# Kernel optimization log

Measured on AMD Instinct MI355X. Metric: run time of the kernel, lower is better.

Reference implementation:

```python
import jax, jax.numpy as jnp
import numpy as np

D = 1024      # neural_dim
M = 8192      # memory_size (assumed fully used)
H = 16        # num_heads
B = 64        # batch
HD = D // H   # head dim


def setup_inputs() -> dict:
    key = jax.random.key(0)
    ks = jax.random.split(key, 24)
    s = 0.02
    inp = {
        "neural_input": jax.random.normal(ks[0], (B, D), jnp.float32),
        "memory_keys": jax.random.normal(ks[1], (M, D), jnp.float32),
        "memory_values": jax.random.normal(ks[2], (M, D), jnp.float32),
        # query/key/value projections (nn.Linear weights are [out, in])
        "Wq": jax.random.normal(ks[3], (D, D), jnp.float32) * s,
        "bq": jnp.zeros((D,), jnp.float32),
        "Wk": jax.random.normal(ks[4], (D, D), jnp.float32) * s,
        "bk": jnp.zeros((D,), jnp.float32),
        "Wv": jax.random.normal(ks[5], (D, D), jnp.float32) * s,
        "bv": jnp.zeros((D,), jnp.float32),
        # MultiheadAttention packed in-projection [3D, D] and out projection
        "in_proj_w": jax.random.normal(ks[6], (3 * D, D), jnp.float32) * s,
        "in_proj_b": jnp.zeros((3 * D,), jnp.float32),
        "out_w": jax.random.normal(ks[7], (D, D), jnp.float32) * s,
        "out_b": jnp.zeros((D,), jnp.float32),
        # memory_gate: Linear(2D->D), ReLU, Linear(D->D), Sigmoid
        "gW1": jax.random.normal(ks[8], (D, 2 * D), jnp.float32) * s,
        "gb1": jnp.zeros((D,), jnp.float32),
        "gW2": jax.random.normal(ks[9], (D, D), jnp.float32) * s,
        "gb2": jnp.zeros((D,), jnp.float32),
        # integration: Linear(2D->2D), ReLU, Linear(2D->D)
        "iW1": jax.random.normal(ks[10], (2 * D, 2 * D), jnp.float32) * s,
        "ib1": jnp.zeros((2 * D,), jnp.float32),
        "iW2": jax.random.normal(ks[11], (D, 2 * D), jnp.float32) * s,
        "ib2": jnp.zeros((D,), jnp.float32),
    }
    return inp


def reference(neural_input, memory_keys, memory_values,
              Wq, bq, Wk, bk, Wv, bv,
              in_proj_w, in_proj_b, out_w, out_b,
              gW1, gb1, gW2, gb2, iW1, ib1, iW2, ib2):
    x = neural_input  # [B, D]
    # pre-projections (memory_used assumed all True -> full tables)
    q = x @ Wq.T + bq                  # [B, D]
    k = memory_keys @ Wk.T + bk        # [M, D]
    v = memory_values @ Wv.T + bv      # [M, D]

    # MultiheadAttention (single query per batch element; K/V shared
    # across batch instead of the redundant expand in the original)
    Wiq, Wik, Wiv = in_proj_w[:D], in_proj_w[D:2 * D], in_proj_w[2 * D:]
    biq, bik, biv = in_proj_b[:D], in_proj_b[D:2 * D], in_proj_b[2 * D:]
    qh = (q @ Wiq.T + biq).reshape(B, H, HD)   # [B, H, hd]
    kh = (k @ Wik.T + bik).reshape(M, H, HD)   # [M, H, hd]
    vh = (v @ Wiv.T + biv).reshape(M, H, HD)   # [M, H, hd]

    scale = 1.0 / np.sqrt(HD).astype(np.float32)
    scores = jnp.einsum('bhd,mhd->bhm', qh, kh) * scale  # [B, H, M]
    attn = jax.nn.softmax(scores, axis=-1)
    ctx = jnp.einsum('bhm,mhd->bhd', attn, vh).reshape(B, D)
    memory_signal = ctx @ out_w.T + out_b      # [B, D]

    # gated fusion
    gate_in = jnp.concatenate([x, memory_signal], axis=-1)          # [B, 2D]
    gate = jax.nn.sigmoid(jax.nn.relu(gate_in @ gW1.T + gb1) @ gW2.T + gb2)
    gated_memory = gate * memory_signal
    combined = jnp.concatenate([x, gated_memory], axis=-1)          # [B, 2D]
    out = jax.nn.relu(combined @ iW1.T + ib1) @ iW2.T + ib2         # [B, D]
    return out
```

## Files before the change

### kernel.cpp

```cpp
#include <hip/hip_runtime.h>
#include <hip/hip_bf16.h>
#include <stdint.h>


typedef __bf16 bf16;
typedef __bf16 bf16x4 __attribute__((ext_vector_type(4)));
typedef __bf16 bf16x8 __attribute__((ext_vector_type(8)));
typedef float f32x4 __attribute__((ext_vector_type(4)));

#define D_ 1024
#define M_ 8192
#define B_ 64
#define H_ 16

static __device__ __forceinline__ void gload16(const void* g, void* l) {
  __builtin_amdgcn_global_load_lds(
      (const __attribute__((address_space(1))) void*)g,
      (__attribute__((address_space(3))) void*)l, 16, 0, 0);
}

static __device__ __forceinline__ f32x4 mfma16(bf16x8 a, bf16x8 b, f32x4 c) {
  return __builtin_amdgcn_mfma_f32_16x16x32_bf16(a, b, c, 0, 0, 0);
}

template <int U, int KLEN, typename OutT>
__device__ __forceinline__ void thin_gemm(
    const bf16* __restrict__ A, int lda,
    const bf16* __restrict__ Bm, int ldb,
    OutT* __restrict__ C, int ldc,
    const float* __restrict__ bias, float scale) {
  const int tid = threadIdx.x, lane = tid & 63, w = tid >> 6;
  const int rl = lane & 15, qq = lane >> 4;
  const bf16* pa = A + (int64_t)(w * 16 + rl) * lda + qq * 8;
  const bf16* pb[4];
  pb[0] = Bm + (int64_t)rl * ldb + qq * 8;
  pb[1] = pb[0] + (int64_t)16 * ldb;
  pb[2] = pb[0] + (int64_t)32 * ldb;
  pb[3] = pb[0] + (int64_t)48 * ldb;
  f32x4 acc[4] = {};
  bf16x8 av[2][U], bv[2][U][4];
#pragma unroll
  for (int u = 0; u < U; u++) {
    av[0][u] = *(const bf16x8*)(pa + u * 32);
#pragma unroll
    for (int j = 0; j < 4; j++)
      bv[0][u][j] = *(const bf16x8*)(pb[j] + u * 32);
  }
  constexpr int NI = KLEN / (32 * U);
#pragma unroll
  for (int it = 0; it < NI; it++) {
    const int cur = it & 1, nxt = cur ^ 1;
    if (it + 1 < NI) {
      int k = (it + 1) * 32 * U;
#pragma unroll
      for (int u = 0; u < U; u++) {
        av[nxt][u] = *(const bf16x8*)(pa + k + u * 32);
#pragma unroll
        for (int j = 0; j < 4; j++)
          bv[nxt][u][j] = *(const bf16x8*)(pb[j] + k + u * 32);
      }
    }
#pragma unroll
    for (int u = 0; u < U; u++)
#pragma unroll
      for (int j = 0; j < 4; j++)
        acc[j] = mfma16(av[cur][u], bv[cur][u][j], acc[j]);
  }
#pragma unroll
  for (int j = 0; j < 4; j++) {
    int gn = j * 16 + rl;
    float bb = bias ? bias[gn] : 0.0f;
#pragma unroll
    for (int r = 0; r < 4; r++) {
      int gm = w * 16 + qq * 4 + r;
      C[(int64_t)gm * ldc + gn] = (OutT)((acc[j][r] + bb) * scale);
    }
  }
}

struct CvtD { const float* src; bf16* dst; int end; };
struct PrepArgs {
  CvtD d[9];
  const float *Wq, *Wk, *Wv, *inw, *inb, *bq, *bk, *bv;
  const float *outb, *gb1, *gb2, *ib1, *ib2;
  bf16* WT;
  float *bc, *msR, *g1R, *gateR, *h1R, *out, *Oraw, *lmat;
};

__global__ __launch_bounds__(256) void prep_kernel(PrepArgs a) {
  const int bx = blockIdx.x, tid = threadIdx.x;
  if (bx < 29760) {
    int g = bx * 256 + tid;
    CvtD dd = a.d[8];
    int begin = a.d[7].end;
#pragma unroll
    for (int t = 7; t >= 0; t--)
      if (g < a.d[t].end) { dd = a.d[t]; begin = t ? a.d[t - 1].end : 0; }
    int i = (g - begin) * 4;
    float4 v = *(const float4*)(dd.src + i);
    bf16x4 o = { (bf16)v.x, (bf16)v.y, (bf16)v.z, (bf16)v.w };
    *(bf16x4*)(dd.dst + i) = o;
  } else if (bx < 32832) {
    int t = bx - 29760;
    int z = t >> 10, rem = t & 1023;
    const float* src = z == 0 ? a.Wq : z == 1 ? a.Wk : a.Wv;
    bf16* out = a.WT + (int64_t)z * D_ * D_;
    __shared__ bf16 tile[32][33];
    int tx = tid & 31, ty = tid >> 5;
    int r0 = (rem >> 5) * 32, c0 = (rem & 31) * 32;
#pragma unroll
    for (int i = 0; i < 32; i += 8)
      tile[ty + i][tx] = (bf16)src[(int64_t)(r0 + ty + i) * D_ + c0 + tx];
    __syncthreads();
#pragma unroll
    for (int i = 0; i < 32; i += 8)
      out[(int64_t)(c0 + ty + i) * D_ + r0 + tx] = tile[tx][ty + i];
  } else if (bx < 33600) {
    int t = bx - 32832;
    int w = tid >> 6, lane = tid & 63;
    int ng = t * 4 + w;
    int z = ng >> 10;
    const float* Wi = a.inw + (int64_t)ng * D_;
    const float* b = z == 0 ? a.bq : z == 1 ? a.bk : a.bv;
    float acc = 0.f;
#pragma unroll
    for (int l = 0; l < D_; l += 64) acc += Wi[l + lane] * b[l + lane];
#pragma unroll
    for (int m = 32; m; m >>= 1) acc += __shfl_xor(acc, m, 64);
    if (lane == 0) a.bc[ng] = acc + a.inb[ng];
  } else if (bx < 33984) {
    int t = bx - 33600;
    int seg = t >> 6, row = t & 63;
    int n = tid * 4;
    const float* b;
    float* dst;
    int bn = n;
    if (seg == 0)      { dst = a.msR   + row * 1024;        b = a.outb; }
    else if (seg == 1) { dst = a.g1R   + row * 1024;        b = a.gb1;  }
    else if (seg == 2) { dst = a.gateR + row * 1024;        b = a.gb2;  }
    else if (seg == 3) { dst = a.h1R   + row * 2048;        b = a.ib1;  }
    else if (seg == 4) { dst = a.h1R   + row * 2048 + 1024; b = a.ib1; bn = 1024 + n; }
    else               { dst = a.out   + row * 1024;        b = a.ib2;  }
    *(float4*)(dst + n) = *(const float4*)(b + bn);
  } else {
    int b = bx - 33984;
    float4 z4 = {0.f, 0.f, 0.f, 0.f};
    *(float4*)(a.Oraw + b * 1024 + tid * 4) = z4;
    if (b < 16 && tid < 64) a.lmat[b * 64 + tid] = 0.f;
  }
}

template <int MODE>
__global__ __launch_bounds__(256) void gemm_big(
    const bf16* __restrict__ A, int lda, int64_t sA,
    const bf16* __restrict__ Bm, int ldb, int64_t sB,
    bf16* __restrict__ C, int ldc, int64_t sC, bf16* __restrict__ Ct,
    const float* __restrict__ bias, int64_t sbias, int K,
    const bf16* __restrict__ qA, const bf16* __restrict__ qB,
    bf16* __restrict__ qC, const float* __restrict__ qbias) {
  int m0, n0, z;
  if (MODE == 0) {
    z = blockIdx.z; m0 = blockIdx.y * 128; n0 = blockIdx.x * 128;
  } else {
    if ((int)blockIdx.x >= 1024) {
      int n0q = ((int)blockIdx.x - 1024) * 64;
      thin_gemm<2, 1024, bf16>(qA, D_, qB + (int64_t)n0q * D_, D_,
                               qC + n0q, D_, qbias + n0q, 0.125f);
      return;
    }
    int lin = blockIdx.x, xcd = lin & 7, slot = lin >> 3;
    z = slot >> 6;
    int r = slot & 63;
    m0 = (xcd * 8 + (r >> 3)) * 128;
    n0 = (r & 7) * 128;
  }
  A += (int64_t)z * sA; Bm += (int64_t)z * sB;
  if (bias) bias += (int64_t)z * sbias;
  __shared__ alignas(16) bf16 As[128 * 32];
  __shared__ alignas(16) bf16 Bs[128 * 32];
  const int tid = threadIdx.x, lane = tid & 63, w = tid >> 6;
  const int wm = (w & 1) * 64, wn = (w >> 1) * 64;
  const int rl = lane & 15, qq = lane >> 4;
  f32x4 acc[4][4] = {};

  int c0 = w * 64 + lane, c1 = (4 + w) * 64 + lane;
  int ra0 = c0 >> 2, qa0 = (c0 & 3) ^ ((ra0 >> 1) & 3);
  int ra1 = c1 >> 2, qa1 = (c1 & 3) ^ ((ra1 >> 1) & 3);
  const bf16* gA0 = A + (int64_t)(m0 + ra0) * lda + qa0 * 8;
  const bf16* gA1 = A + (int64_t)(m0 + ra1) * lda + qa1 * 8;
  const bf16* gB0 = Bm + (int64_t)(n0 + ra0) * ldb + qa0 * 8;
  const bf16* gB1 = Bm + (int64_t)(n0 + ra1) * ldb + qa1 * 8;
  bf16* lA0 = As + w * 512;
  bf16* lA1 = As + (4 + w) * 512;
  bf16* lB0 = Bs + w * 512;
  bf16* lB1 = Bs + (4 + w) * 512;

  for (int k0 = 0; k0 < K; k0 += 32) {
    __syncthreads();
    gload16(gA0 + k0, lA0);
    gload16(gA1 + k0, lA1);
    gload16(gB0 + k0, lB0);
    gload16(gB1 + k0, lB1);
    __syncthreads();
    bf16x8 af[4], bb[4];
#pragma unroll
    for (int i = 0; i < 4; i++) {
      int r = wm + i * 16 + rl;
      af[i] = *(const bf16x8*)(As + r * 32 + (qq ^ ((r >> 1) & 3)) * 8);
    }
#pragma unroll
    for (int j = 0; j < 4; j++) {
      int r = wn + j * 16 + rl;
      bb[j] = *(const bf16x8*)(Bs + r * 32 + (qq ^ ((r >> 1) & 3)) * 8);
    }
#pragma unroll
    for (int i = 0; i < 4; i++)
#pragma unroll
      for (int j = 0; j < 4; j++)
        acc[i][j] = mfma16(af[i], bb[j], acc[i][j]);
  }
  if (MODE == 1 && z == 1) {
#pragma unroll
    for (int j = 0; j < 4; j++) {
      int gn = n0 + wn + j * 16 + rl;
      float bb2 = bias ? bias[gn] : 0.0f;
#pragma unroll
      for (int i = 0; i < 4; i++) {
        int gm0 = m0 + wm + i * 16 + qq * 4;
        f32x4 a = acc[i][j];
        bf16x4 o = { (bf16)(a[0] + bb2), (bf16)(a[1] + bb2),
                     (bf16)(a[2] + bb2), (bf16)(a[3] + bb2) };
        *(bf16x4*)(Ct + (int64_t)gn * M_ + gm0) = o;
      }
    }
  } else {
    C += (int64_t)z * sC;
#pragma unroll
    for (int j = 0; j < 4; j++) {
      int gn = n0 + wn + j * 16 + rl;
      float bb2 = bias ? bias[gn] : 0.0f;
#pragma unroll
      for (int i = 0; i < 4; i++) {
        int gm0 = m0 + wm + i * 16 + qq * 4;
#pragma unroll
        for (int r = 0; r < 4; r++)
          C[(int64_t)(gm0 + r) * ldc + gn] = (bf16)(acc[i][j][r] + bb2);
      }
    }
  }
}

__global__ __launch_bounds__(512) void gemm256(
    const bf16* __restrict__ A,
    const bf16* __restrict__ Wc,
    const float* __restrict__ bc,
    bf16* __restrict__ kh, bf16* __restrict__ vhT,
    const bf16* __restrict__ qA, const bf16* __restrict__ qB,
    bf16* __restrict__ qC, const float* __restrict__ qbias) {
  extern __shared__ __align__(16) bf16 lds[];
  const int bid = blockIdx.x;
  if (bid >= 256) {
    if (threadIdx.x < 256) {
      int n0q = (bid - 256) * 64;
      thin_gemm<2, 1024, bf16>(qA, D_, qB + (int64_t)n0q * D_, D_,
                               qC + n0q, D_, qbias + n0q, 0.125f);
    }
    return;
  }
  const int lin = bid;
  const int xcd = lin & 7, s = lin >> 3;
  const int z = xcd >> 2;
  const int m0 = ((xcd & 3) * 8 + (s >> 2)) * 256;
  const int n0 = (s & 3) * 256;
  const bf16* Ab = A + (int64_t)z * M_ * D_;
  const bf16* Bb = Wc + (int64_t)(z + 1) * D_ * D_;
  const float* bias = bc + (z + 1) * D_;

  const int tid = threadIdx.x, lane = tid & 63, w = tid >> 6;
  const int rl = lane & 15, qq = lane >> 4;
  const int wr = w >> 2, wcn = w & 3;

  const int ci0 = w * 128 + lane, ci1 = ci0 + 64;
  const int ra0 = ci0 >> 2, ca0 = (ci0 & 3) ^ ((ra0 >> 1) & 3);
  const int ra1 = ci1 >> 2, ca1 = (ci1 & 3) ^ ((ra1 >> 1) & 3);
  const bf16* gA0 = Ab + (int64_t)(m0 + ra0) * D_ + ca0 * 8;
  const bf16* gA1 = Ab + (int64_t)(m0 + ra1) * D_ + ca1 * 8;
  const bf16* gB0 = Bb + (int64_t)(n0 + ra0) * D_ + ca0 * 8;
  const bf16* gB1 = Bb + (int64_t)(n0 + ra1) * D_ + ca1 * 8;
  const int lA0 = w * 1024, lA1 = lA0 + 512;

  f32x4 acc[8][4] = {};
  bf16x8 bfr[4], afr[4];
  const int sq8 = (qq ^ ((rl >> 1) & 3)) * 8;

#define SCB __builtin_amdgcn_sched_barrier(0)
#define BARR __builtin_amdgcn_s_barrier()
#define VMW(N) asm volatile("s_waitcnt vmcnt(" #N ")")

#define STAGE_FULL(BUF, KT)                          \
  do {                                               \
    bf16* bse_ = lds + (BUF) * 16384;                \
    gload16(gA0 + (KT) * 32, bse_ + lA0);            \
    gload16(gA1 + (KT) * 32, bse_ + lA1);            \
    gload16(gB0 + (KT) * 32, bse_ + 8192 + lA0);     \
    gload16(gB1 + (KT) * 32, bse_ + 8192 + lA1);     \
  } while (0)

#define PH_A(BUF, DOSTAGE, SKT)                                              \
  do {                                                                       \
    const bf16* ba_ = lds + (BUF) * 16384;                                   \
    const bf16* bb_ = ba_ + 8192;                                            \
    for (int j = 0; j < 4; j++)                                              \
      bfr[j] = *(const bf16x8*)(bb_ + (wcn * 64 + j * 16 + rl) * 32 + sq8);  \
    for (int mi = 0; mi < 4; mi++)                                           \
      afr[mi] = *(const bf16x8*)(ba_ + (wr * 128 + mi * 16 + rl) * 32 + sq8);\
    if (DOSTAGE) {                                                           \
      bf16* bse_ = lds + ((SKT) & 3) * 16384;                                \
      gload16(gA0 + (SKT) * 32, bse_ + lA0);                                 \
      gload16(gA1 + (SKT) * 32, bse_ + lA1);                                 \
    }                                                                        \
    SCB; BARR; SCB;                                                          \
    __builtin_amdgcn_s_setprio(1);                                           \
    for (int mi = 0; mi < 4; mi++)                                           \
      for (int j = 0; j < 4; j++)                                            \
        acc[mi][j] = mfma16(afr[mi], bfr[j], acc[mi][j]);                    \
    __builtin_amdgcn_s_setprio(0);                                           \
    SCB; BARR; SCB;                                                          \
  } while (0)

#define PH_B(BUF, DOSTAGE, SKT, VMSTMT)                                      \
  do {                                                                       \
    const bf16* ba_ = lds + (BUF) * 16384;                                   \
    for (int mi = 0; mi < 4; mi++)                                           \
      afr[mi] =                                                              \
          *(const bf16x8*)(ba_ + (wr * 128 + (mi + 4) * 16 + rl) * 32 + sq8);\
    if (DOSTAGE) {                                                           \
      bf16* bse_ = lds + ((SKT) & 3) * 16384;                                \
      gload16(gB0 + (SKT) * 32, bse_ + 8192 + lA0);                          \
      gload16(gB1 + (SKT) * 32, bse_ + 8192 + lA1);                          \
    }                                                                        \
    VMSTMT;                                                                  \
    SCB; BARR; SCB;                                                          \
    __builtin_amdgcn_s_setprio(1);                                           \
    for (int mi = 0; mi < 4; mi++)                                           \
      for (int j = 0; j < 4; j++)                                            \
        acc[mi + 4][j] = mfma16(afr[mi], bfr[j], acc[mi + 4][j]);            \
    __builtin_amdgcn_s_setprio(0);                                           \
    SCB; BARR; SCB;                                                          \
  } while (0)

  STAGE_FULL(0, 0);
  STAGE_FULL(1, 1);
  STAGE_FULL(2, 2);
  VMW(8);
  SCB; BARR; SCB;

#pragma unroll 1
  for (int t = 0; t < 7; t++) {
    const int kb = t * 4;
    PH_A(0, 1, kb + 3); PH_B(0, 1, kb + 3, VMW(8));
    PH_A(1, 1, kb + 4); PH_B(1, 1, kb + 4, VMW(8));
    PH_A(2, 1, kb + 5); PH_B(2, 1, kb + 5, VMW(8));
    PH_A(3, 1, kb + 6); PH_B(3, 1, kb + 6, VMW(8));
  }
  PH_A(0, 1, 31); PH_B(0, 1, 31, VMW(8));
  PH_A(1, 0, 0);  PH_B(1, 0, 0, VMW(4));
  PH_A(2, 0, 0);  PH_B(2, 0, 0, VMW(0));
  PH_A(3, 0, 0);  PH_B(3, 0, 0, (void)0);

#undef SCB
#undef BARR
#undef VMW
#undef STAGE_FULL
#undef PH_A
#undef PH_B

  if (z == 0) {
#pragma unroll
    for (int j = 0; j < 4; j++) {
      int gn = n0 + wcn * 64 + j * 16 + rl;
      float bb2 = bias[gn];
#pragma unroll
      for (int mi = 0; mi < 8; mi++) {
        int gm0 = m0 + wr * 128 + mi * 16 + qq * 4;
#pragma unroll
        for (int r = 0; r < 4; r++)
          kh[(int64_t)(gm0 + r) * D_ + gn] = (bf16)(acc[mi][j][r] + bb2);
      }
    }
  } else {
#pragma unroll
    for (int j = 0; j < 4; j++) {
      int gn = n0 + wcn * 64 + j * 16 + rl;
      float bb2 = bias[gn];
#pragma unroll
      for (int mi = 0; mi < 8; mi++) {
        int gm0 = m0 + wr * 128 + mi * 16 + qq * 4;
        f32x4 a = acc[mi][j];
        bf16x4 o = { (bf16)(a[0] + bb2), (bf16)(a[1] + bb2),
                     (bf16)(a[2] + bb2), (bf16)(a[3] + bb2) };
        *(bf16x4*)(vhT + (int64_t)gn * M_ + gm0) = o;
      }
    }
  }
}

__global__ __launch_bounds__(256, 2) void flash_kernel(
    const bf16* __restrict__ qh, const bf16* __restrict__ kh,
    const bf16* __restrict__ vhT, float* __restrict__ Oraw,
    float* __restrict__ lmat) {
  const int tid = threadIdx.x, lane = tid & 63, w = tid >> 6;
  const int rl = lane & 15, qq = lane >> 4;
  const int h = blockIdx.x >> 4, c = blockIdx.x & 15;
  __shared__ alignas(16) bf16 Plds[4 * 16 * 72];
  const bf16* qhp = qh + (int64_t)(w * 16 + rl) * D_ + h * 64 + qq * 8;
  bf16x8 aq0 = *(const bf16x8*)(qhp);
  bf16x8 aq1 = *(const bf16x8*)(qhp + 32);
  float lsum[4] = {0.f, 0.f, 0.f, 0.f};
  f32x4 acc_o[4] = {};
  bf16* pl = Plds + w * 1152;
  const bf16* khb = kh + (int64_t)(c * 512) * D_ + h * 64 + qq * 8;
  const bf16* vtb = vhT + (int64_t)(h * 64) * M_ + c * 512 + qq * 8;
  for (int nt = 0; nt < 8; nt++) {
    int mb = nt * 64;
    bf16x8 bk0[4], bk1[4], vv0[4], vv1[4];
#pragma unroll
    for (int j = 0; j < 4; j++) {
      const bf16* p = khb + (int64_t)(mb + j * 16 + rl) * D_;
      bk0[j] = *(const bf16x8*)(p);
      bk1[j] = *(const bf16x8*)(p + 32);
      const bf16* q = vtb + (int64_t)(j * 16 + rl) * M_ + mb;
      vv0[j] = *(const bf16x8*)(q);
      vv1[j] = *(const bf16x8*)(q + 32);
    }
    f32x4 s[4] = {};
#pragma unroll
    for (int j = 0; j < 4; j++) {
      s[j] = mfma16(aq0, bk0[j], s[j]);
      s[j] = mfma16(aq1, bk1[j], s[j]);
    }
#pragma unroll
    for (int j = 0; j < 4; j++)
#pragma unroll
      for (int r = 0; r < 4; r++) {
        float p = __expf(s[j][r]);
        lsum[r] += p;
        pl[(qq * 4 + r) * 72 + j * 16 + rl] = (bf16)p;
      }
    bf16x8 pa0 = *(const bf16x8*)(pl + rl * 72 + qq * 8);
    bf16x8 pa1 = *(const bf16x8*)(pl + rl * 72 + 32 + qq * 8);
#pragma unroll
    for (int j = 0; j < 4; j++) {
      acc_o[j] = mfma16(pa0, vv0[j], acc_o[j]);
      acc_o[j] = mfma16(pa1, vv1[j], acc_o[j]);
    }
  }
#pragma unroll
  for (int msk = 1; msk <= 8; msk <<= 1)
#pragma unroll
    for (int r = 0; r < 4; r++) lsum[r] += __shfl_xor(lsum[r], msk, 64);
#pragma unroll
  for (int j = 0; j < 4; j++)
#pragma unroll
    for (int r = 0; r < 4; r++)
      atomicAdd(&Oraw[(int64_t)(w * 16 + qq * 4 + r) * D_ + h * 64 + j * 16 + rl],
                acc_o[j][r]);
  if (rl == 0)
#pragma unroll
    for (int r = 0; r < 4; r++)
      atomicAdd(&lmat[h * 64 + w * 16 + qq * 4 + r], lsum[r]);
}

struct Chunk { const void* p0; const void* p1; int ld; int kind; };
struct StageArgs { Chunk c[16]; };

template <int NKK>
__global__ __launch_bounds__(256) void tail_stage(
    StageArgs sa, const bf16* __restrict__ Bw, int ldb,
    float* __restrict__ Craw, int ldc) {
  const int n0 = blockIdx.x * 64, kc = blockIdx.y;
  const int bk0 = kc * NKK * 32;
  const Chunk ch = sa.c[kc];
  const int tid = threadIdx.x, lane = tid & 63, w = tid >> 6;
  const int rl = lane & 15, qq = lane >> 4;
  const int m = w * 16 + rl;
  const bf16* pb[4];
#pragma unroll
  for (int j = 0; j < 4; j++)
    pb[j] = Bw + (int64_t)(n0 + j * 16 + rl) * ldb + bk0 + qq * 8;
  f32x4 acc[4] = {};
#pragma unroll
  for (int kk = 0; kk < NKK; kk++) {
    bf16x8 af;
    if (ch.kind == 0) {
      af = *(const bf16x8*)((const bf16*)ch.p0 + (int64_t)m * ch.ld +
                            kk * 32 + qq * 8);
    } else {
      const float* p = (const float*)ch.p0 + (int64_t)m * ch.ld + kk * 32 + qq * 8;
      float4 u0 = *(const float4*)p;
      float4 u1 = *(const float4*)(p + 4);
      if (ch.kind == 2) {
        u0.x = fmaxf(u0.x, 0.f); u0.y = fmaxf(u0.y, 0.f);
        u0.z = fmaxf(u0.z, 0.f); u0.w = fmaxf(u0.w, 0.f);
        u1.x = fmaxf(u1.x, 0.f); u1.y = fmaxf(u1.y, 0.f);
        u1.z = fmaxf(u1.z, 0.f); u1.w = fmaxf(u1.w, 0.f);
      } else if (ch.kind == 3) {
        const float* pm = (const float*)ch.p1 + (int64_t)m * ch.ld + kk * 32 + qq * 8;
        float4 m0 = *(const float4*)pm;
        float4 m1 = *(const float4*)(pm + 4);
        u0.x = m0.x / (1.f + __expf(-u0.x)); u0.y = m0.y / (1.f + __expf(-u0.y));
        u0.z = m0.z / (1.f + __expf(-u0.z)); u0.w = m0.w / (1.f + __expf(-u0.w));
        u1.x = m1.x / (1.f + __expf(-u1.x)); u1.y = m1.y / (1.f + __expf(-u1.y));
        u1.z = m1.z / (1.f + __expf(-u1.z)); u1.w = m1.w / (1.f + __expf(-u1.w));
      } else if (ch.kind == 4) {
        int hidx = (bk0 + kk * 32) >> 6;
        float linv = 1.0f / ((const float*)ch.p1)[hidx * 64 + m];
        u0.x *= linv; u0.y *= linv; u0.z *= linv; u0.w *= linv;
        u1.x *= linv; u1.y *= linv; u1.z *= linv; u1.w *= linv;
      }
      af = (bf16x8){ (bf16)u0.x, (bf16)u0.y, (bf16)u0.z, (bf16)u0.w,
                     (bf16)u1.x, (bf16)u1.y, (bf16)u1.z, (bf16)u1.w };
    }
    bf16x8 bf_[4];
#pragma unroll
    for (int j = 0; j < 4; j++) bf_[j] = *(const bf16x8*)(pb[j] + kk * 32);
#pragma unroll
    for (int j = 0; j < 4; j++) acc[j] = mfma16(af, bf_[j], acc[j]);
  }
#pragma unroll
  for (int j = 0; j < 4; j++) {
    int gn = n0 + j * 16 + rl;
#pragma unroll
    for (int r = 0; r < 4; r++) {
      int gm = w * 16 + qq * 4 + r;
      atomicAdd(&Craw[(int64_t)gm * ldc + gn], acc[j][r]);
    }
  }
}

extern "C" void kernel_launch(void* const* d_in, const int* in_sizes, int n_in,
                              void* d_out, int out_size, void* d_ws,
                              size_t ws_size, hipStream_t stream) {
  (void)in_sizes; (void)n_in; (void)out_size;
  const float* x    = (const float*)d_in[0];
  const float* mk   = (const float*)d_in[1];
  const float* mv   = (const float*)d_in[2];
  const float* Wq   = (const float*)d_in[3];
  const float* bq   = (const float*)d_in[4];
  const float* Wk   = (const float*)d_in[5];
  const float* bk   = (const float*)d_in[6];
  const float* Wv   = (const float*)d_in[7];
  const float* bv   = (const float*)d_in[8];
  const float* inw  = (const float*)d_in[9];
  const float* inb  = (const float*)d_in[10];
  const float* outw = (const float*)d_in[11];
  const float* outb = (const float*)d_in[12];
  const float* gW1  = (const float*)d_in[13];
  const float* gb1  = (const float*)d_in[14];
  const float* gW2  = (const float*)d_in[15];
  const float* gb2  = (const float*)d_in[16];
  const float* iW1  = (const float*)d_in[17];
  const float* ib1  = (const float*)d_in[18];
  const float* iW2  = (const float*)d_in[19];
  const float* ib2  = (const float*)d_in[20];

  char* ws = (char*)d_ws;
  size_t off = 0;
  auto alloc = [&](size_t bytes) {
    char* p = ws + off;
    off += (bytes + 255) & ~(size_t)255;
    return p;
  };
  bf16* mkmv  = (bf16*)alloc((size_t)2 * M_ * D_ * 2);
  bf16* inpj  = (bf16*)alloc((size_t)3 * D_ * D_ * 2);
  bf16* WT    = (bf16*)alloc((size_t)3 * D_ * D_ * 2);
  bf16* Wc    = (bf16*)alloc((size_t)3 * D_ * D_ * 2);
  float* bc   = (float*)alloc(3 * D_ * 4);
  bf16* xbf   = (bf16*)alloc((size_t)B_ * D_ * 2);
  bf16* qh    = (bf16*)alloc((size_t)B_ * D_ * 2);
  bf16* kh    = (bf16*)alloc((size_t)M_ * D_ * 2);
  bf16* vhT   = (bf16*)alloc((size_t)M_ * D_ * 2);
  float* Oraw = (float*)alloc((size_t)B_ * D_ * 4);
  float* lmat = (float*)alloc((size_t)H_ * B_ * 4);
  float* msR  = (float*)alloc((size_t)B_ * D_ * 4);
  float* g1R  = (float*)alloc((size_t)B_ * D_ * 4);
  float* gateR= (float*)alloc((size_t)B_ * D_ * 4);
  float* h1R  = (float*)alloc((size_t)B_ * 2 * D_ * 4);
  bf16* gW1b  = (bf16*)alloc((size_t)D_ * 2 * D_ * 2);
  bf16* gW2b  = (bf16*)alloc((size_t)D_ * D_ * 2);
  bf16* iW1b  = (bf16*)alloc((size_t)2 * D_ * 2 * D_ * 2);
  bf16* iW2b  = (bf16*)alloc((size_t)D_ * 2 * D_ * 2);
  bf16* outwb = (bf16*)alloc((size_t)D_ * D_ * 2);
  if (ws_size < off) return;

  PrepArgs pa;
  pa.d[0] = { mk,   mkmv,           2097152 };
  pa.d[1] = { mv,   mkmv + M_ * D_, 4194304 };
  pa.d[2] = { inw,  inpj,           4980736 };
  pa.d[3] = { gW1,  gW1b,           5505024 };
  pa.d[4] = { gW2,  gW2b,           5767168 };
  pa.d[5] = { iW1,  iW1b,           6815744 };
  pa.d[6] = { iW2,  iW2b,           7340032 };
  pa.d[7] = { outw, outwb,          7602176 };
  pa.d[8] = { x,    xbf,            7618560 };
  pa.Wq = Wq; pa.Wk = Wk; pa.Wv = Wv; pa.inw = inw; pa.inb = inb;
  pa.bq = bq; pa.bk = bk; pa.bv = bv;
  pa.outb = outb; pa.gb1 = gb1; pa.gb2 = gb2; pa.ib1 = ib1; pa.ib2 = ib2;
  pa.WT = WT; pa.bc = bc; pa.msR = msR; pa.g1R = g1R; pa.gateR = gateR;
  pa.h1R = h1R; pa.out = (float*)d_out; pa.Oraw = Oraw; pa.lmat = lmat;
  prep_kernel<<<dim3(34048), 256, 0, stream>>>(pa);

  gemm_big<0><<<dim3(8, 8, 3), 256, 0, stream>>>(
      inpj, D_, (int64_t)D_ * D_, WT, D_, (int64_t)D_ * D_,
      Wc, D_, (int64_t)D_ * D_, nullptr, nullptr, 0, D_,
      nullptr, nullptr, nullptr, nullptr);

  hipFuncSetAttribute((const void*)gemm256,
                      hipFuncAttributeMaxDynamicSharedMemorySize, 131072);
  gemm256<<<dim3(272), dim3(512), 131072, stream>>>(
      mkmv, Wc, bc, kh, vhT, xbf, Wc, qh, bc);

  flash_kernel<<<dim3(256), 256, 0, stream>>>(qh, kh, vhT, Oraw, lmat);

  StageArgs s1;
  for (int kc = 0; kc < 8; kc++) s1.c[kc] = { Oraw + kc * 128, lmat, D_, 4 };
  tail_stage<4><<<dim3(16, 8), 256, 0, stream>>>(s1, outwb, D_, msR, D_);

  StageArgs s2;
  for (int kc = 0; kc < 8; kc++)  s2.c[kc] = { xbf + kc * 128, nullptr, D_, 0 };
  for (int kc = 8; kc < 16; kc++) s2.c[kc] = { msR + (kc - 8) * 128, nullptr, D_, 1 };
  tail_stage<4><<<dim3(16, 16), 256, 0, stream>>>(s2, gW1b, 2 * D_, g1R, D_);

  StageArgs s3;
  for (int kc = 0; kc < 8; kc++) s3.c[kc] = { g1R + kc * 128, nullptr, D_, 2 };
  tail_stage<4><<<dim3(16, 8), 256, 0, stream>>>(s3, gW2b, D_, gateR, D_);

  StageArgs s4;
  for (int kc = 0; kc < 8; kc++)  s4.c[kc] = { xbf + kc * 128, nullptr, D_, 0 };
  for (int kc = 8; kc < 16; kc++)
    s4.c[kc] = { gateR + (kc - 8) * 128, msR + (kc - 8) * 128, D_, 3 };
  tail_stage<4><<<dim3(32, 16), 256, 0, stream>>>(s4, iW1b, 2 * D_, h1R, 2 * D_);

  StageArgs s5;
  for (int kc = 0; kc < 16; kc++) s5.c[kc] = { h1R + kc * 128, nullptr, 2 * D_, 2 };
  tail_stage<4><<<dim3(16, 16), 256, 0, stream>>>(s5, iW2b, 2 * D_,
                                                  (float*)d_out, D_);
}
```

Baseline: 343.5 us.

## Fuse five tail GEMV stages into one kernel with flag-based inter-stage dependencies

Replaces five separate tail_stage launches with a single tail_fused kernel. Blocks are assigned to stages by block index and wait on global atomic counters that the producing stage increments with release semantics. Weights are preloaded into registers before spinning, so weight fetch overlaps the wait on the previous stage. The prep kernel conversion loop also now handles 16 elements per thread instead of 4, cutting its block count. The gain relies on lower launch overhead and on overlapping stages. The spin-wait assumes earlier stages' blocks are scheduled ahead of later ones, which risks deadlock if later-stage blocks fill the GPU first; the launch order is ascending block index, so this is likely but not guaranteed.

After: 552.7 us. 1.61x slower.

```diff
diff --git a/kernel.cpp b/kernel.cpp
--- a/kernel.cpp
+++ b/kernel.cpp
@@ -85,23 +85,27 @@
   const float *outb, *gb1, *gb2, *ib1, *ib2;
   bf16* WT;
   float *bc, *msR, *g1R, *gateR, *h1R, *out, *Oraw, *lmat;
+  uint32_t* flags;
 };
 
 __global__ __launch_bounds__(256) void prep_kernel(PrepArgs a) {
   const int bx = blockIdx.x, tid = threadIdx.x;
-  if (bx < 29760) {
+  if (bx < 7440) {
     int g = bx * 256 + tid;
     CvtD dd = a.d[8];
     int begin = a.d[7].end;
 #pragma unroll
     for (int t = 7; t >= 0; t--)
       if (g < a.d[t].end) { dd = a.d[t]; begin = t ? a.d[t - 1].end : 0; }
-    int i = (g - begin) * 4;
-    float4 v = *(const float4*)(dd.src + i);
-    bf16x4 o = { (bf16)v.x, (bf16)v.y, (bf16)v.z, (bf16)v.w };
-    *(bf16x4*)(dd.dst + i) = o;
-  } else if (bx < 32832) {
-    int t = bx - 29760;
+    int i = (g - begin) * 16;
+#pragma unroll
+    for (int u = 0; u < 4; u++) {
+      float4 v = *(const float4*)(dd.src + i + u * 4);
+      bf16x4 o = { (bf16)v.x, (bf16)v.y, (bf16)v.z, (bf16)v.w };
+      *(bf16x4*)(dd.dst + i + u * 4) = o;
+    }
+  } else if (bx < 10512) {
+    int t = bx - 7440;
     int z = t >> 10, rem = t & 1023;
     const float* src = z == 0 ? a.Wq : z == 1 ? a.Wk : a.Wv;
     bf16* out = a.WT + (int64_t)z * D_ * D_;
@@ -115,8 +119,8 @@
 #pragma unroll
     for (int i = 0; i < 32; i += 8)
       out[(int64_t)(c0 + ty + i) * D_ + r0 + tx] = tile[tx][ty + i];
-  } else if (bx < 33600) {
-    int t = bx - 32832;
+  } else if (bx < 11280) {
+    int t = bx - 10512;
     int w = tid >> 6, lane = tid & 63;
     int ng = t * 4 + w;
     int z = ng >> 10;
@@ -128,8 +132,8 @@
 #pragma unroll
     for (int m = 32; m; m >>= 1) acc += __shfl_xor(acc, m, 64);
     if (lane == 0) a.bc[ng] = acc + a.inb[ng];
-  } else if (bx < 33984) {
-    int t = bx - 33600;
+  } else if (bx < 11664) {
+    int t = bx - 11280;
     int seg = t >> 6, row = t & 63;
     int n = tid * 4;
     const float* b;
@@ -143,10 +147,11 @@
     else               { dst = a.out   + row * 1024;        b = a.ib2;  }
     *(float4*)(dst + n) = *(const float4*)(b + bn);
   } else {
-    int b = bx - 33984;
+    int b = bx - 11664;
     float4 z4 = {0.f, 0.f, 0.f, 0.f};
     *(float4*)(a.Oraw + b * 1024 + tid * 4) = z4;
     if (b < 16 && tid < 64) a.lmat[b * 64 + tid] = 0.f;
+    if (b == 0 && tid < 16) a.flags[tid] = 0u;
   }
 }
 
@@ -471,61 +476,116 @@
       atomicAdd(&lmat[h * 64 + w * 16 + qq * 4 + r], lsum[r]);
 }
 
-struct Chunk { const void* p0; const void* p1; int ld; int kind; };
-struct StageArgs { Chunk c[16]; };
-
-template <int NKK>
-__global__ __launch_bounds__(256) void tail_stage(
-    StageArgs sa, const bf16* __restrict__ Bw, int ldb,
-    float* __restrict__ Craw, int ldc) {
-  const int n0 = blockIdx.x * 64, kc = blockIdx.y;
-  const int bk0 = kc * NKK * 32;
-  const Chunk ch = sa.c[kc];
+__global__ __launch_bounds__(256, 5) void tail_fused(
+    const float* __restrict__ Oraw, const float* __restrict__ lmat,
+    const bf16* __restrict__ xbf, float* __restrict__ msR,
+    float* __restrict__ g1R, float* __restrict__ gateR,
+    float* __restrict__ h1R, float* __restrict__ out,
+    const bf16* __restrict__ outwb, const bf16* __restrict__ gW1b,
+    const bf16* __restrict__ gW2b, const bf16* __restrict__ iW1b,
+    const bf16* __restrict__ iW2b, uint32_t* __restrict__ flags) {
+  const int bid = blockIdx.x;
   const int tid = threadIdx.x, lane = tid & 63, w = tid >> 6;
   const int rl = lane & 15, qq = lane >> 4;
   const int m = w * 16 + rl;
+
+  int stage, local;
+  if (bid < 128)       { stage = 0; local = bid; }
+  else if (bid < 384)  { stage = 1; local = bid - 128; }
+  else if (bid < 512)  { stage = 2; local = bid - 384; }
+  else if (bid < 1024) { stage = 3; local = bid - 512; }
+  else                 { stage = 4; local = bid - 1024; }
+
+  int n0, kc;
+  if (stage == 3) { n0 = (local & 31) * 64; kc = local >> 5; }
+  else            { n0 = (local & 15) * 64; kc = local >> 4; }
+  const int bk0 = kc * 128;
+
+  const bf16* Bw; int ldb; float* Craw; int ldc;
+  const float* p0f = nullptr; const bf16* p0b = nullptr;
+  const float* p1f = nullptr; int lda; int kind;
+  int spin = -1, starget = 0, sig;
+  switch (stage) {
+    case 0:
+      Bw = outwb; ldb = D_; Craw = msR; ldc = D_;
+      p0f = Oraw + bk0; p1f = lmat; lda = D_; kind = 4; sig = 0;
+      break;
+    case 1:
+      Bw = gW1b; ldb = 2 * D_; Craw = g1R; ldc = D_; sig = 1;
+      if (kc < 8) { p0b = xbf + bk0; lda = D_; kind = 0; }
+      else { p0f = msR + (kc - 8) * 128; lda = D_; kind = 1;
+             spin = 0; starget = 128; }
+      break;
+    case 2:
+      Bw = gW2b; ldb = D_; Craw = gateR; ldc = D_;
+      p0f = g1R + bk0; lda = D_; kind = 2; spin = 1; starget = 256; sig = 2;
+      break;
+    case 3:
+      Bw = iW1b; ldb = 2 * D_; Craw = h1R; ldc = 2 * D_; sig = 3;
+      if (kc < 8) { p0b = xbf + bk0; lda = D_; kind = 0; }
+      else { p0f = gateR + (kc - 8) * 128; p1f = msR + (kc - 8) * 128;
+             lda = D_; kind = 3; spin = 2; starget = 128; }
+      break;
+    default:
+      Bw = iW2b; ldb = 2 * D_; Craw = out; ldc = D_;
+      p0f = h1R + bk0; lda = 2 * D_; kind = 2; spin = 3; starget = 512;
+      sig = -1;
+      break;
+  }
+
   const bf16* pb[4];
 #pragma unroll
   for (int j = 0; j < 4; j++)
     pb[j] = Bw + (int64_t)(n0 + j * 16 + rl) * ldb + bk0 + qq * 8;
+  bf16x8 bw[4][4];
+#pragma unroll
+  for (int kk = 0; kk < 4; kk++)
+#pragma unroll
+    for (int j = 0; j < 4; j++) bw[kk][j] = *(const bf16x8*)(pb[j] + kk * 32);
+
+  if (spin >= 0) {
+    if (tid == 0) {
+      while (__hip_atomic_load(&flags[spin], __ATOMIC_ACQUIRE,
+                               __HIP_MEMORY_SCOPE_AGENT) < (uint32_t)starget)
+        __builtin_amdgcn_s_sleep(2);
+    }
+    __syncthreads();
+  }
+
   f32x4 acc[4] = {};
 #pragma unroll
-  for (int kk = 0; kk < NKK; kk++) {
+  for (int kk = 0; kk < 4; kk++) {
     bf16x8 af;
-    if (ch.kind == 0) {
-      af = *(const bf16x8*)((const bf16*)ch.p0 + (int64_t)m * ch.ld +
-                            kk * 32 + qq * 8);
+    if (kind == 0) {
+      af = *(const bf16x8*)(p0b + (int64_t)m * lda + kk * 32 + qq * 8);
     } else {
-      const float* p = (const float*)ch.p0 + (int64_t)m * ch.ld + kk * 32 + qq * 8;
+      const float* p = p0f + (int64_t)m * lda + kk * 32 + qq * 8;
       float4 u0 = *(const float4*)p;
       float4 u1 = *(const float4*)(p + 4);
-      if (ch.kind == 2) {
+      if (kind == 2) {
         u0.x = fmaxf(u0.x, 0.f); u0.y = fmaxf(u0.y, 0.f);
         u0.z = fmaxf(u0.z, 0.f); u0.w = fmaxf(u0.w, 0.f);
         u1.x = fmaxf(u1.x, 0.f); u1.y = fmaxf(u1.y, 0.f);
         u1.z = fmaxf(u1.z, 0.f); u1.w = fmaxf(u1.w, 0.f);
-      } else if (ch.kind == 3) {
-        const float* pm = (const float*)ch.p1 + (int64_t)m * ch.ld + kk * 32 + qq * 8;
+      } else if (kind == 3) {
+        const float* pm = p1f + (int64_t)m * lda + kk * 32 + qq * 8;
         float4 m0 = *(const float4*)pm;
         float4 m1 = *(const float4*)(pm + 4);
         u0.x = m0.x / (1.f + __expf(-u0.x)); u0.y = m0.y / (1.f + __expf(-u0.y));
         u0.z = m0.z / (1.f + __expf(-u0.z)); u0.w = m0.w / (1.f + __expf(-u0.w));
         u1.x = m1.x / (1.f + __expf(-u1.x)); u1.y = m1.y / (1.f + __expf(-u1.y));
         u1.z = m1.z / (1.f + __expf(-u1.z)); u1.w = m1.w / (1.f + __expf(-u1.w));
-      } else if (ch.kind == 4) {
+      } else if (kind == 4) {
         int hidx = (bk0 + kk * 32) >> 6;
-        float linv = 1.0f / ((const float*)ch.p1)[hidx * 64 + m];
+        float linv = 1.0f / p1f[hidx * 64 + m];
         u0.x *= linv; u0.y *= linv; u0.z *= linv; u0.w *= linv;
         u1.x *= linv; u1.y *= linv; u1.z *= linv; u1.w *= linv;
       }
       af = (bf16x8){ (bf16)u0.x, (bf16)u0.y, (bf16)u0.z, (bf16)u0.w,
                      (bf16)u1.x, (bf16)u1.y, (bf16)u1.z, (bf16)u1.w };
     }
-    bf16x8 bf_[4];
-#pragma unroll
-    for (int j = 0; j < 4; j++) bf_[j] = *(const bf16x8*)(pb[j] + kk * 32);
-#pragma unroll
-    for (int j = 0; j < 4; j++) acc[j] = mfma16(af, bf_[j], acc[j]);
+#pragma unroll
+    for (int j = 0; j < 4; j++) acc[j] = mfma16(af, bw[kk][j], acc[j]);
   }
 #pragma unroll
   for (int j = 0; j < 4; j++) {
@@ -535,6 +595,12 @@
       int gm = w * 16 + qq * 4 + r;
       atomicAdd(&Craw[(int64_t)gm * ldc + gn], acc[j][r]);
     }
+  }
+  if (sig >= 0) {
+    __syncthreads();
+    if (tid == 0)
+      __hip_atomic_fetch_add(&flags[sig], 1u, __ATOMIC_RELEASE,
+                             __HIP_MEMORY_SCOPE_AGENT);
   }
 }
 
@@ -591,24 +657,26 @@
   bf16* iW1b  = (bf16*)alloc((size_t)2 * D_ * 2 * D_ * 2);
   bf16* iW2b  = (bf16*)alloc((size_t)D_ * 2 * D_ * 2);
   bf16* outwb = (bf16*)alloc((size_t)D_ * D_ * 2);
+  uint32_t* flags = (uint32_t*)alloc(64);
   if (ws_size < off) return;
 
   PrepArgs pa;
-  pa.d[0] = { mk,   mkmv,           2097152 };
-  pa.d[1] = { mv,   mkmv + M_ * D_, 4194304 };
-  pa.d[2] = { inw,  inpj,           4980736 };
-  pa.d[3] = { gW1,  gW1b,           5505024 };
-  pa.d[4] = { gW2,  gW2b,           5767168 };
-  pa.d[5] = { iW1,  iW1b,           6815744 };
-  pa.d[6] = { iW2,  iW2b,           7340032 };
-  pa.d[7] = { outw, outwb,          7602176 };
-  pa.d[8] = { x,    xbf,            7618560 };
+  pa.d[0] = { mk,   mkmv,           524288 };
+  pa.d[1] = { mv,   mkmv + M_ * D_, 1048576 };
+  pa.d[2] = { inw,  inpj,           1245184 };
+  pa.d[3] = { gW1,  gW1b,           1376256 };
+  pa.d[4] = { gW2,  gW2b,           1441792 };
+  pa.d[5] = { iW1,  iW1b,           1703936 };
+  pa.d[6] = { iW2,  iW2b,           1835008 };
+  pa.d[7] = { outw, outwb,          1900544 };
+  pa.d[8] = { x,    xbf,            1904640 };
   pa.Wq = Wq; pa.Wk = Wk; pa.Wv = Wv; pa.inw = inw; pa.inb = inb;
   pa.bq = bq; pa.bk = bk; pa.bv = bv;
   pa.outb = outb; pa.gb1 = gb1; pa.gb2 = gb2; pa.ib1 = ib1; pa.ib2 = ib2;
   pa.WT = WT; pa.bc = bc; pa.msR = msR; pa.g1R = g1R; pa.gateR = gateR;
   pa.h1R = h1R; pa.out = (float*)d_out; pa.Oraw = Oraw; pa.lmat = lmat;
-  prep_kernel<<<dim3(34048), 256, 0, stream>>>(pa);
+  pa.flags = flags;
+  prep_kernel<<<dim3(11728), 256, 0, stream>>>(pa);
 
   gemm_big<0><<<dim3(8, 8, 3), 256, 0, stream>>>(
       inpj, D_, (int64_t)D_ * D_, WT, D_, (int64_t)D_ * D_,
@@ -622,27 +690,7 @@
 
   flash_kernel<<<dim3(256), 256, 0, stream>>>(qh, kh, vhT, Oraw, lmat);
 
-  StageArgs s1;
-  for (int kc = 0; kc < 8; kc++) s1.c[kc] = { Oraw + kc * 128, lmat, D_, 4 };
-  tail_stage<4><<<dim3(16, 8), 256, 0, stream>>>(s1, outwb, D_, msR, D_);
-
-  StageArgs s2;
-  for (int kc = 0; kc < 8; kc++)  s2.c[kc] = { xbf + kc * 128, nullptr, D_, 0 };
-  for (int kc = 8; kc < 16; kc++) s2.c[kc] = { msR + (kc - 8) * 128, nullptr, D_, 1 };
-  tail_stage<4><<<dim3(16, 16), 256, 0, stream>>>(s2, gW1b, 2 * D_, g1R, D_);
-
-  StageArgs s3;
-  for (int kc = 0; kc < 8; kc++) s3.c[kc] = { g1R + kc * 128, nullptr, D_, 2 };
-  tail_stage<4><<<dim3(16, 8), 256, 0, stream>>>(s3, gW2b, D_, gateR, D_);
-
-  StageArgs s4;
-  for (int kc = 0; kc < 8; kc++)  s4.c[kc] = { xbf + kc * 128, nullptr, D_, 0 };
-  for (int kc = 8; kc < 16; kc++)
-    s4.c[kc] = { gateR + (kc - 8) * 128, msR + (kc - 8) * 128, D_, 3 };
-  tail_stage<4><<<dim3(32, 16), 256, 0, stream>>>(s4, iW1b, 2 * D_, h1R, 2 * D_);
-
-  StageArgs s5;
-  for (int kc = 0; kc < 16; kc++) s5.c[kc] = { h1R + kc * 128, nullptr, 2 * D_, 2 };
-  tail_stage<4><<<dim3(16, 16), 256, 0, stream>>>(s5, iW2b, 2 * D_,
-                                                  (float*)d_out, D_);
-}
+  tail_fused<<<dim3(1280), 256, 0, stream>>>(
+      Oraw, lmat, xbf, msR, g1R, gateR, h1R, (float*)d_out,
+      outwb, gW1b, gW2b, iW1b, iW2b, flags);
+}
```

## Split-K weight-combine GEMM and reassociate query path through Wq

Applied to the files above, without the earlier changes.

The weight-combining GEMM for the key and value paths now runs split-K over four chunks into fp32 partials, which a new kernel sums and converts to bf16. This gives 512 blocks instead of 192. The query path no longer builds a combined Wq weight. It computes x@Wq^T as a thin GEMM fused into the same launch, then applies the in-projection inside gemm256, so the 1024x1024x1024 product for q is skipped. The prep conversion also handles 16 elements per thread to cut block count. The cost is an extra launch and fp32 partial traffic, which borrows the kh buffer as scratch.

Measured after the change: 360.0 us. +4.8%, slower.

```diff
diff --git a/kernel.cpp b/kernel.cpp
--- a/kernel.cpp
+++ b/kernel.cpp
@@ -80,8 +80,8 @@
 
 struct CvtD { const float* src; bf16* dst; int end; };
 struct PrepArgs {
-  CvtD d[9];
-  const float *Wq, *Wk, *Wv, *inw, *inb, *bq, *bk, *bv;
+  CvtD d[10];
+  const float *Wk, *Wv, *inw, *inb, *bq, *bk, *bv;
   const float *outb, *gb1, *gb2, *ib1, *ib2;
   bf16* WT;
   float *bc, *msR, *g1R, *gateR, *h1R, *out, *Oraw, *lmat;
@@ -89,22 +89,25 @@
 
 __global__ __launch_bounds__(256) void prep_kernel(PrepArgs a) {
   const int bx = blockIdx.x, tid = threadIdx.x;
-  if (bx < 29760) {
+  if (bx < 7696) {
     int g = bx * 256 + tid;
-    CvtD dd = a.d[8];
-    int begin = a.d[7].end;
-#pragma unroll
-    for (int t = 7; t >= 0; t--)
+    CvtD dd = a.d[9];
+    int begin = a.d[8].end;
+#pragma unroll
+    for (int t = 8; t >= 0; t--)
       if (g < a.d[t].end) { dd = a.d[t]; begin = t ? a.d[t - 1].end : 0; }
-    int i = (g - begin) * 4;
-    float4 v = *(const float4*)(dd.src + i);
-    bf16x4 o = { (bf16)v.x, (bf16)v.y, (bf16)v.z, (bf16)v.w };
-    *(bf16x4*)(dd.dst + i) = o;
-  } else if (bx < 32832) {
-    int t = bx - 29760;
+    int i = (g - begin) * 16;
+#pragma unroll
+    for (int u = 0; u < 4; u++) {
+      float4 v = *(const float4*)(dd.src + i + u * 4);
+      bf16x4 o = { (bf16)v.x, (bf16)v.y, (bf16)v.z, (bf16)v.w };
+      *(bf16x4*)(dd.dst + i + u * 4) = o;
+    }
+  } else if (bx < 9744) {
+    int t = bx - 7696;
     int z = t >> 10, rem = t & 1023;
-    const float* src = z == 0 ? a.Wq : z == 1 ? a.Wk : a.Wv;
-    bf16* out = a.WT + (int64_t)z * D_ * D_;
+    const float* src = z == 0 ? a.Wk : a.Wv;
+    bf16* out = a.WT + (int64_t)(z + 1) * D_ * D_;
     __shared__ bf16 tile[32][33];
     int tx = tid & 31, ty = tid >> 5;
     int r0 = (rem >> 5) * 32, c0 = (rem & 31) * 32;
@@ -115,8 +118,8 @@
 #pragma unroll
     for (int i = 0; i < 32; i += 8)
       out[(int64_t)(c0 + ty + i) * D_ + r0 + tx] = tile[tx][ty + i];
-  } else if (bx < 33600) {
-    int t = bx - 32832;
+  } else if (bx < 10512) {
+    int t = bx - 9744;
     int w = tid >> 6, lane = tid & 63;
     int ng = t * 4 + w;
     int z = ng >> 10;
@@ -128,8 +131,8 @@
 #pragma unroll
     for (int m = 32; m; m >>= 1) acc += __shfl_xor(acc, m, 64);
     if (lane == 0) a.bc[ng] = acc + a.inb[ng];
-  } else if (bx < 33984) {
-    int t = bx - 33600;
+  } else if (bx < 10896) {
+    int t = bx - 10512;
     int seg = t >> 6, row = t & 63;
     int n = tid * 4;
     const float* b;
@@ -143,39 +146,34 @@
     else               { dst = a.out   + row * 1024;        b = a.ib2;  }
     *(float4*)(dst + n) = *(const float4*)(b + bn);
   } else {
-    int b = bx - 33984;
+    int b = bx - 10896;
     float4 z4 = {0.f, 0.f, 0.f, 0.f};
     *(float4*)(a.Oraw + b * 1024 + tid * 4) = z4;
     if (b < 16 && tid < 64) a.lmat[b * 64 + tid] = 0.f;
   }
 }
 
-template <int MODE>
-__global__ __launch_bounds__(256) void gemm_big(
-    const bf16* __restrict__ A, int lda, int64_t sA,
-    const bf16* __restrict__ Bm, int ldb, int64_t sB,
-    bf16* __restrict__ C, int ldc, int64_t sC, bf16* __restrict__ Ct,
-    const float* __restrict__ bias, int64_t sbias, int K,
-    const bf16* __restrict__ qA, const bf16* __restrict__ qB,
-    bf16* __restrict__ qC, const float* __restrict__ qbias) {
-  int m0, n0, z;
-  if (MODE == 0) {
-    z = blockIdx.z; m0 = blockIdx.y * 128; n0 = blockIdx.x * 128;
-  } else {
-    if ((int)blockIdx.x >= 1024) {
-      int n0q = ((int)blockIdx.x - 1024) * 64;
-      thin_gemm<2, 1024, bf16>(qA, D_, qB + (int64_t)n0q * D_, D_,
-                               qC + n0q, D_, qbias + n0q, 0.125f);
-      return;
-    }
-    int lin = blockIdx.x, xcd = lin & 7, slot = lin >> 3;
-    z = slot >> 6;
-    int r = slot & 63;
-    m0 = (xcd * 8 + (r >> 3)) * 128;
-    n0 = (r & 7) * 128;
-  }
-  A += (int64_t)z * sA; Bm += (int64_t)z * sB;
-  if (bias) bias += (int64_t)z * sbias;
+__global__ __launch_bounds__(256) void gemm_l2(
+    const bf16* __restrict__ inpj,
+    const bf16* __restrict__ WT,
+    float* __restrict__ Wcp,
+    const bf16* __restrict__ xbf, const bf16* __restrict__ Wqb,
+    bf16* __restrict__ q1) {
+  const int bid = blockIdx.x;
+  if (bid >= 512) {
+    int n0q = (bid - 512) * 64;
+    thin_gemm<2, 1024, bf16>(xbf, D_, Wqb + (int64_t)n0q * D_, D_,
+                             q1 + n0q, D_, nullptr, 1.0f);
+    return;
+  }
+  const int n0 = (bid & 7) * 128;
+  const int m0 = ((bid >> 3) & 7) * 128;
+  const int zc = bid >> 6;
+  const int z = zc >> 2, kc = zc & 3;
+  const bf16* A = inpj + (int64_t)(z + 1) * D_ * D_ + kc * 256;
+  const bf16* Bm = WT + (int64_t)(z + 1) * D_ * D_ + kc * 256;
+  float* C = Wcp + (int64_t)zc * D_ * D_;
+
   __shared__ alignas(16) bf16 As[128 * 32];
   __shared__ alignas(16) bf16 Bs[128 * 32];
   const int tid = threadIdx.x, lane = tid & 63, w = tid >> 6;
@@ -186,16 +184,16 @@
   int c0 = w * 64 + lane, c1 = (4 + w) * 64 + lane;
   int ra0 = c0 >> 2, qa0 = (c0 & 3) ^ ((ra0 >> 1) & 3);
   int ra1 = c1 >> 2, qa1 = (c1 & 3) ^ ((ra1 >> 1) & 3);
-  const bf16* gA0 = A + (int64_t)(m0 + ra0) * lda + qa0 * 8;
-  const bf16* gA1 = A + (int64_t)(m0 + ra1) * lda + qa1 * 8;
-  const bf16* gB0 = Bm + (int64_t)(n0 + ra0) * ldb + qa0 * 8;
-  const bf16* gB1 = Bm + (int64_t)(n0 + ra1) * ldb + qa1 * 8;
+  const bf16* gA0 = A + (int64_t)(m0 + ra0) * D_ + qa0 * 8;
+  const bf16* gA1 = A + (int64_t)(m0 + ra1) * D_ + qa1 * 8;
+  const bf16* gB0 = Bm + (int64_t)(n0 + ra0) * D_ + qa0 * 8;
+  const bf16* gB1 = Bm + (int64_t)(n0 + ra1) * D_ + qa1 * 8;
   bf16* lA0 = As + w * 512;
   bf16* lA1 = As + (4 + w) * 512;
   bf16* lB0 = Bs + w * 512;
   bf16* lB1 = Bs + (4 + w) * 512;
 
-  for (int k0 = 0; k0 < K; k0 += 32) {
+  for (int k0 = 0; k0 < 256; k0 += 32) {
     __syncthreads();
     gload16(gA0 + k0, lA0);
     gload16(gA1 + k0, lA1);
@@ -219,35 +217,32 @@
       for (int j = 0; j < 4; j++)
         acc[i][j] = mfma16(af[i], bb[j], acc[i][j]);
   }
-  if (MODE == 1 && z == 1) {
-#pragma unroll
-    for (int j = 0; j < 4; j++) {
-      int gn = n0 + wn + j * 16 + rl;
-      float bb2 = bias ? bias[gn] : 0.0f;
-#pragma unroll
-      for (int i = 0; i < 4; i++) {
-        int gm0 = m0 + wm + i * 16 + qq * 4;
-        f32x4 a = acc[i][j];
-        bf16x4 o = { (bf16)(a[0] + bb2), (bf16)(a[1] + bb2),
-                     (bf16)(a[2] + bb2), (bf16)(a[3] + bb2) };
-        *(bf16x4*)(Ct + (int64_t)gn * M_ + gm0) = o;
-      }
-    }
-  } else {
-    C += (int64_t)z * sC;
-#pragma unroll
-    for (int j = 0; j < 4; j++) {
-      int gn = n0 + wn + j * 16 + rl;
-      float bb2 = bias ? bias[gn] : 0.0f;
-#pragma unroll
-      for (int i = 0; i < 4; i++) {
-        int gm0 = m0 + wm + i * 16 + qq * 4;
-#pragma unroll
-        for (int r = 0; r < 4; r++)
-          C[(int64_t)(gm0 + r) * ldc + gn] = (bf16)(acc[i][j][r] + bb2);
-      }
-    }
-  }
+#pragma unroll
+  for (int j = 0; j < 4; j++) {
+    int gn = n0 + wn + j * 16 + rl;
+#pragma unroll
+    for (int i = 0; i < 4; i++) {
+      int gm0 = m0 + wm + i * 16 + qq * 4;
+#pragma unroll
+      for (int r = 0; r < 4; r++)
+        C[(int64_t)(gm0 + r) * D_ + gn] = acc[i][j][r];
+    }
+  }
+}
+
+__global__ __launch_bounds__(256) void cvt_wc(
+    const float* __restrict__ Wcp, bf16* __restrict__ Wc) {
+  const int z = blockIdx.x >> 10, b = blockIdx.x & 1023;
+  const int i = (b * 256 + threadIdx.x) * 4;
+  const float* p = Wcp + (int64_t)(z * 4) * D_ * D_ + i;
+  float4 s = *(const float4*)p;
+#pragma unroll
+  for (int kc = 1; kc < 4; kc++) {
+    float4 t = *(const float4*)(p + (int64_t)kc * D_ * D_);
+    s.x += t.x; s.y += t.y; s.z += t.z; s.w += t.w;
+  }
+  bf16x4 o = { (bf16)s.x, (bf16)s.y, (bf16)s.z, (bf16)s.w };
+  *(bf16x4*)(Wc + (int64_t)(z + 1) * D_ * D_ + i) = o;
 }
 
 __global__ __launch_bounds__(512) void gemm256(
@@ -591,34 +586,37 @@
   bf16* iW1b  = (bf16*)alloc((size_t)2 * D_ * 2 * D_ * 2);
   bf16* iW2b  = (bf16*)alloc((size_t)D_ * 2 * D_ * 2);
   bf16* outwb = (bf16*)alloc((size_t)D_ * D_ * 2);
+  bf16* Wqb   = (bf16*)alloc((size_t)D_ * D_ * 2);
+  bf16* q1    = (bf16*)alloc((size_t)B_ * D_ * 2);
   if (ws_size < off) return;
+  float* Wcp = (float*)kh;
 
   PrepArgs pa;
-  pa.d[0] = { mk,   mkmv,           2097152 };
-  pa.d[1] = { mv,   mkmv + M_ * D_, 4194304 };
-  pa.d[2] = { inw,  inpj,           4980736 };
-  pa.d[3] = { gW1,  gW1b,           5505024 };
-  pa.d[4] = { gW2,  gW2b,           5767168 };
-  pa.d[5] = { iW1,  iW1b,           6815744 };
-  pa.d[6] = { iW2,  iW2b,           7340032 };
-  pa.d[7] = { outw, outwb,          7602176 };
-  pa.d[8] = { x,    xbf,            7618560 };
-  pa.Wq = Wq; pa.Wk = Wk; pa.Wv = Wv; pa.inw = inw; pa.inb = inb;
+  pa.d[0] = { mk,   mkmv,           524288 };
+  pa.d[1] = { mv,   mkmv + M_ * D_, 1048576 };
+  pa.d[2] = { inw,  inpj,           1245184 };
+  pa.d[3] = { gW1,  gW1b,           1376256 };
+  pa.d[4] = { gW2,  gW2b,           1441792 };
+  pa.d[5] = { iW1,  iW1b,           1703936 };
+  pa.d[6] = { iW2,  iW2b,           1835008 };
+  pa.d[7] = { outw, outwb,          1900544 };
+  pa.d[8] = { Wq,   Wqb,            1966080 };
+  pa.d[9] = { x,    xbf,            1970176 };
+  pa.Wk = Wk; pa.Wv = Wv; pa.inw = inw; pa.inb = inb;
   pa.bq = bq; pa.bk = bk; pa.bv = bv;
   pa.outb = outb; pa.gb1 = gb1; pa.gb2 = gb2; pa.ib1 = ib1; pa.ib2 = ib2;
   pa.WT = WT; pa.bc = bc; pa.msR = msR; pa.g1R = g1R; pa.gateR = gateR;
   pa.h1R = h1R; pa.out = (float*)d_out; pa.Oraw = Oraw; pa.lmat = lmat;
-  prep_kernel<<<dim3(34048), 256, 0, stream>>>(pa);
-
-  gemm_big<0><<<dim3(8, 8, 3), 256, 0, stream>>>(
-      inpj, D_, (int64_t)D_ * D_, WT, D_, (int64_t)D_ * D_,
-      Wc, D_, (int64_t)D_ * D_, nullptr, nullptr, 0, D_,
-      nullptr, nullptr, nullptr, nullptr);
+  prep_kernel<<<dim3(10960), 256, 0, stream>>>(pa);
+
+  gemm_l2<<<dim3(528), 256, 0, stream>>>(inpj, WT, Wcp, xbf, Wqb, q1);
+
+  cvt_wc<<<dim3(2048), 256, 0, stream>>>(Wcp, Wc);
 
   hipFuncSetAttribute((const void*)gemm256,
                       hipFuncAttributeMaxDynamicSharedMemorySize, 131072);
   gemm256<<<dim3(272), dim3(512), 131072, stream>>>(
-      mkmv, Wc, bc, kh, vhT, xbf, Wc, qh, bc);
+      mkmv, Wc, bc, kh, vhT, q1, inpj, qh, bc);
 
   flash_kernel<<<dim3(256), 256, 0, stream>>>(qh, kh, vhT, Oraw, lmat);
 
```
